# Kernel tuning notes

Measured on AMD Instinct MI355X. Metric: run time of the kernel, lower is better.

## Reference

```python
import jax, jax.numpy as jnp
import numpy as np

B, LQ, LK, D = 8, 2048, 2048, 64
TEMPERATURE = 8.0  # sqrt(D)


def setup_inputs() -> dict:
    key = jax.random.key(0)
    ks = jax.random.split(key, 9)
    q = jax.random.normal(ks[0], (B, LQ, D), dtype=jnp.float32)
    k = jax.random.normal(ks[1], (B, LK, D), dtype=jnp.float32)
    v = jax.random.normal(ks[2], (B, LK, D), dtype=jnp.float32)
    mask = jax.random.randint(ks[3], (B, LQ, LK), 0, 2).astype(jnp.bool_)
    f1 = jax.random.normal(ks[4], (B, LQ, LK), dtype=jnp.float32)
    f2 = jax.random.normal(ks[5], (B, LQ, LK), dtype=jnp.float32)
    f3 = jax.random.normal(ks[6], (B, LQ, LK), dtype=jnp.float32)
    f4 = jax.random.normal(ks[7], (B, LQ, LK), dtype=jnp.float32)
    f5 = jax.random.normal(ks[8], (B, LQ, LK), dtype=jnp.float32)
    return {"q": q, "k": k, "v": v, "mask": mask,
            "tf_f1_features": f1, "tf_f2_features": f2, "tf_f3_features": f3,
            "tf_f4_features": f4, "tf_f5_features": f5}


def reference(q, k, v, mask, tf_f1_features, tf_f2_features, tf_f3_features,
              tf_f4_features, tf_f5_features):
    # scores: [B, Lq, Lk]
    attn = jnp.einsum("bqd,bkd->bqk", q, k)
    attn = attn + tf_f1_features + tf_f2_features + tf_f3_features + tf_f4_features + tf_f5_features
    attn = attn / TEMPERATURE
    attn = jnp.where(mask, -jnp.inf, attn)
    attn = jax.nn.softmax(attn, axis=2)
    # dropout is identity (attn_dropout=0 / eval mode)
    output = jnp.einsum("bqk,bkd->bqd", attn, v)
    return (output, attn)
```

## Files before the change

kernel.cpp:

```cpp
#include <hip/hip_runtime.h>


#define BBn 8
#define LQn 2048
#define LKn 2048
#define DDn 64

typedef _Float16 half8 __attribute__((ext_vector_type(8)));
typedef _Float16 half4 __attribute__((ext_vector_type(4)));
typedef float floatx4 __attribute__((ext_vector_type(4)));
typedef int intx4 __attribute__((ext_vector_type(4)));

__global__ __launch_bounds__(256) void prep_all(
    const float* __restrict__ kp, const float* __restrict__ vp,
    const unsigned* __restrict__ m, _Float16* __restrict__ kh,
    _Float16* __restrict__ vh, int* __restrict__ flag) {
  const int blk = blockIdx.x;
  const int tid = threadIdx.x;
  if (blk < 512) {
    const size_t off = ((size_t)blk * 256 + tid) * 8;
    floatx4 x0 = *(const floatx4*)(kp + off);
    floatx4 x1 = *(const floatx4*)(kp + off + 4);
    half8 h;
#pragma unroll
    for (int i = 0; i < 4; ++i) { h[i] = (_Float16)x0[i]; h[i + 4] = (_Float16)x1[i]; }
    *(half8*)(kh + off) = h;
  } else if (blk < 1024) {
    int fid = (blk - 512) * 256 + tid;
    const int lr  = fid & 15;  fid >>= 4;
    const int lgp = fid & 3;   fid >>= 2;
    const int dt  = fid & 3;   fid >>= 2;
    const int tc  = fid & 1;   fid >>= 1;
    const int kb6 = fid & 31;  fid >>= 5;
    const int b   = fid;
    const float* vbase =
        vp + ((size_t)(b * LKn + kb6 * 64 + tc * 32 + lgp * 8)) * DDn + dt * 16 + lr;
    half8 h;
#pragma unroll
    for (int i = 0; i < 8; ++i) h[i] = (_Float16)vbase[i * DDn];
    const size_t vof =
        ((((((size_t)b * 32 + kb6) * 2 + tc) * 4 + dt) * 4 + lgp) * 16 + lr) * 8;
    *(half8*)(vh + vof) = h;
  } else {
    __shared__ int s_int, s_f32;
    if (tid == 0) { s_int = 1; s_f32 = 1; }
    __syncthreads();
    int oki = 1, okf = 1;
    for (int i = tid; i < 4096; i += 256) {
      unsigned x = m[i];
      oki &= (x <= 1u);
      okf &= (x == 0u || x == 0x3f800000u);
    }
    atomicAnd(&s_int, oki);
    atomicAnd(&s_f32, okf);
    __syncthreads();
    if (tid == 0) *flag = s_int ? 0 : (s_f32 ? 1 : 2);
  }
}

__global__ __launch_bounds__(256) void detect_mask(const unsigned* __restrict__ m,
                                                   int* __restrict__ flag) {
  __shared__ int s_int, s_f32;
  const int tid = threadIdx.x;
  if (tid == 0) { s_int = 1; s_f32 = 1; }
  __syncthreads();
  int oki = 1, okf = 1;
  for (int i = tid; i < 4096; i += 256) {
    unsigned x = m[i];
    oki &= (x <= 1u);
    okf &= (x == 0u || x == 0x3f800000u);
  }
  atomicAnd(&s_int, oki);
  atomicAnd(&s_f32, okf);
  __syncthreads();
  if (tid == 0) *flag = s_int ? 0 : (s_f32 ? 1 : 2);
}

__global__ __launch_bounds__(512, 4) void attn_logits32(
    const float* __restrict__ qp, const _Float16* __restrict__ kh,
    const float* __restrict__ f1, const float* __restrict__ f2,
    const float* __restrict__ f3, const float* __restrict__ f4,
    const float* __restrict__ f5,
    const void* __restrict__ maskp, const int* __restrict__ flag,
    float* __restrict__ attn, float* __restrict__ invl) {
  const int blk = blockIdx.x;
  const int b   = blk >> 6;
  const int q0  = (blk & 63) << 5;
  const int tid = threadIdx.x;
  const int w   = tid >> 6;
  const int l   = tid & 63;
  const int lr  = l & 15;
  const int lgp = l >> 4;
  const int mode = *flag;

  half8 aq[2][2];
#pragma unroll
  for (int t = 0; t < 2; ++t) {
    const float* qrow = qp + ((size_t)(b * LQn + q0 + t * 16 + lr)) * DDn;
#pragma unroll
    for (int dc = 0; dc < 2; ++dc) {
      floatx4 x0 = *(const floatx4*)(qrow + dc * 32 + lgp * 8);
      floatx4 x1 = *(const floatx4*)(qrow + dc * 32 + lgp * 8 + 4);
      half8 h;
#pragma unroll
      for (int i = 0; i < 4; ++i) { h[i] = (_Float16)x0[i]; h[i + 4] = (_Float16)x1[i]; }
      aq[t][dc] = h;
    }
  }

  float lsum[2][4] = {{0.f, 0.f, 0.f, 0.f}, {0.f, 0.f, 0.f, 0.f}};
  const size_t rowbase = (size_t)b * LQn + q0;
  const int t0 = w * 256;

  for (int kb = t0; kb < t0 + 256; kb += 64) {
    floatx4 acc[2][4];
#pragma unroll
    for (int t = 0; t < 2; ++t)
#pragma unroll
      for (int jj = 0; jj < 4; ++jj) acc[t][jj] = (floatx4){0.f, 0.f, 0.f, 0.f};
#pragma unroll
    for (int dc = 0; dc < 2; ++dc) {
#pragma unroll
      for (int jj = 0; jj < 4; ++jj) {
        half8 bk = *(const half8*)(
            kh + ((size_t)(b * LKn + kb + 4 * lr + jj)) * DDn + dc * 32 + lgp * 8);
#pragma unroll
        for (int t = 0; t < 2; ++t)
          acc[t][jj] = __builtin_amdgcn_mfma_f32_16x16x32_f16(aq[t][dc], bk, acc[t][jj], 0, 0, 0);
      }
    }
#pragma unroll
    for (int t = 0; t < 2; ++t) {
#pragma unroll
      for (int r = 0; r < 4; ++r) {
        const int row = t * 16 + lgp * 4 + r;
        const size_t fof = (rowbase + row) * (size_t)LKn + (size_t)(kb + 4 * lr);
        floatx4 v1 = *(const floatx4*)(f1 + fof);
        floatx4 v2 = *(const floatx4*)(f2 + fof);
        floatx4 v3 = *(const floatx4*)(f3 + fof);
        floatx4 v4 = *(const floatx4*)(f4 + fof);
        floatx4 v5 = *(const floatx4*)(f5 + fof);
        int msk[4];
        if (mode == 0) {
          intx4 m4 = *(const intx4*)((const int*)maskp + fof);
          msk[0] = (m4[0] != 0); msk[1] = (m4[1] != 0);
          msk[2] = (m4[2] != 0); msk[3] = (m4[3] != 0);
        } else if (mode == 1) {
          floatx4 m4 = *(const floatx4*)((const float*)maskp + fof);
          msk[0] = (m4[0] != 0.f); msk[1] = (m4[1] != 0.f);
          msk[2] = (m4[2] != 0.f); msk[3] = (m4[3] != 0.f);
        } else {
          unsigned mv = *(const unsigned*)((const unsigned char*)maskp + fof);
          msk[0] = (int)(mv & 0xffu); msk[1] = (int)((mv >> 8) & 0xffu);
          msk[2] = (int)((mv >> 16) & 0xffu); msk[3] = (int)((mv >> 24) & 0xffu);
        }
        floatx4 ev;
#pragma unroll
        for (int jj = 0; jj < 4; ++jj) {
          float lgt = (acc[t][jj][r] + v1[jj] + v2[jj] + v3[jj] + v4[jj] + v5[jj]) * 0.125f;
          float e = msk[jj] ? 0.f : __expf(lgt - 16.f);
          ev[jj] = e;
          lsum[t][r] += e;
        }
        *(floatx4*)(attn + fof) = ev;
      }
    }
  }

#pragma unroll
  for (int off = 1; off < 16; off <<= 1) {
#pragma unroll
    for (int t = 0; t < 2; ++t)
#pragma unroll
      for (int r = 0; r < 4; ++r) lsum[t][r] += __shfl_xor(lsum[t][r], off);
  }
  __shared__ float lds_l[8][32];
  if (lr == 0) {
#pragma unroll
    for (int t = 0; t < 2; ++t)
#pragma unroll
      for (int r = 0; r < 4; ++r) lds_l[w][t * 16 + lgp * 4 + r] = lsum[t][r];
  }
  __syncthreads();
  if (tid < 32) {
    float s = 0.f;
#pragma unroll
    for (int ww = 0; ww < 8; ++ww) s += lds_l[ww][tid];
    invl[rowbase + tid] = 1.0f / s;
  }
}

__global__ __launch_bounds__(256, 4) void attn_pv(
    const _Float16* __restrict__ vh, const float* __restrict__ invl,
    float* __restrict__ attn, float* __restrict__ outp) {
  const int blk = blockIdx.x;
  const int b   = blk >> 7;
  const int q0  = (blk & 127) << 4;
  const int tid = threadIdx.x;
  const int w   = tid >> 6;
  const int l   = tid & 63;
  const int lr  = l & 15;
  const int lgp = l >> 4;

  __shared__ __align__(16) _Float16 p16[4][16][72];
  __shared__ float osum[4][16][64];

  const size_t rowbase = (size_t)b * LQn + q0;
  float il[4];
#pragma unroll
  for (int r = 0; r < 4; ++r) il[r] = invl[rowbase + lgp * 4 + r];

  floatx4 acc[4];
#pragma unroll
  for (int dt = 0; dt < 4; ++dt) acc[dt] = (floatx4){0.f, 0.f, 0.f, 0.f};

  const int t0 = w * 512;
  for (int kb = t0; kb < t0 + 512; kb += 64) {
    const int kb6 = kb >> 6;
#pragma unroll
    for (int r = 0; r < 4; ++r) {
      const int row = lgp * 4 + r;
      const size_t fof = (rowbase + row) * (size_t)LKn + (size_t)(kb + 4 * lr);
      floatx4 e = *(const floatx4*)(attn + fof);
      floatx4 p = e * il[r];
      *(floatx4*)(attn + fof) = p;
      half4 hp;
#pragma unroll
      for (int jj = 0; jj < 4; ++jj) hp[jj] = (_Float16)p[jj];
      *(half4*)(&p16[w][row][4 * lr]) = hp;
    }
    half8 pa[2];
#pragma unroll
    for (int tc = 0; tc < 2; ++tc)
      pa[tc] = *(const half8*)(&p16[w][lr][tc * 32 + lgp * 8]);
#pragma unroll
    for (int tc = 0; tc < 2; ++tc) {
#pragma unroll
      for (int dt = 0; dt < 4; ++dt) {
        half8 bv = *(const half8*)(
            vh + ((((((size_t)b * 32 + kb6) * 2 + tc) * 4 + dt) * 4 + lgp) * 16 + lr) * 8);
        acc[dt] = __builtin_amdgcn_mfma_f32_16x16x32_f16(pa[tc], bv, acc[dt], 0, 0, 0);
      }
    }
  }

#pragma unroll
  for (int dt = 0; dt < 4; ++dt) {
#pragma unroll
    for (int r = 0; r < 4; ++r) osum[w][lgp * 4 + r][dt * 16 + lr] = acc[dt][r];
  }
  __syncthreads();
#pragma unroll
  for (int ii = 0; ii < 4; ++ii) {
    int idx = tid + 256 * ii;
    int row = idx >> 6, d = idx & 63;
    float s = osum[0][row][d] + osum[1][row][d] + osum[2][row][d] + osum[3][row][d];
    outp[(rowbase + row) * DDn + d] = s;
  }
}

__global__ __launch_bounds__(512, 4) void attn_logits_fb(
    const float* __restrict__ qp, const float* __restrict__ kp,
    const float* __restrict__ f1, const float* __restrict__ f2,
    const float* __restrict__ f3, const float* __restrict__ f4,
    const float* __restrict__ f5,
    const void* __restrict__ maskp, const int* __restrict__ flag,
    float* __restrict__ attn, float* __restrict__ invl) {
  const int blk = blockIdx.x;
  const int b   = blk >> 7;
  const int q0  = (blk & 127) << 4;
  const int tid = threadIdx.x;
  const int w   = tid >> 6;
  const int l   = tid & 63;
  const int lr  = l & 15;
  const int lgp = l >> 4;
  const int mode = *flag;
  const float* qrow = qp + ((size_t)(b * LQn + q0 + lr)) * DDn;
  half8 aq[2];
#pragma unroll
  for (int dc = 0; dc < 2; ++dc) {
    floatx4 x0 = *(const floatx4*)(qrow + dc * 32 + lgp * 8);
    floatx4 x1 = *(const floatx4*)(qrow + dc * 32 + lgp * 8 + 4);
    half8 h;
#pragma unroll
    for (int i = 0; i < 4; ++i) { h[i] = (_Float16)x0[i]; h[i + 4] = (_Float16)x1[i]; }
    aq[dc] = h;
  }
  float lsum[4] = {0.f, 0.f, 0.f, 0.f};
  const size_t rowbase = (size_t)b * LQn + q0;
  const int t0 = w * 256;
  for (int kb = t0; kb < t0 + 256; kb += 64) {
    floatx4 acc[4];
#pragma unroll
    for (int jj = 0; jj < 4; ++jj) acc[jj] = (floatx4){0.f, 0.f, 0.f, 0.f};
#pragma unroll
    for (int dc = 0; dc < 2; ++dc) {
#pragma unroll
      for (int jj = 0; jj < 4; ++jj) {
        const float* krow =
            kp + ((size_t)(b * LKn + kb + 4 * lr + jj)) * DDn + dc * 32 + lgp * 8;
        floatx4 x0 = *(const floatx4*)(krow);
        floatx4 x1 = *(const floatx4*)(krow + 4);
        half8 h;
#pragma unroll
        for (int i = 0; i < 4; ++i) { h[i] = (_Float16)x0[i]; h[i + 4] = (_Float16)x1[i]; }
        acc[jj] = __builtin_amdgcn_mfma_f32_16x16x32_f16(aq[dc], h, acc[jj], 0, 0, 0);
      }
    }
#pragma unroll
    for (int r = 0; r < 4; ++r) {
      const int row = lgp * 4 + r;
      const size_t fof = (rowbase + row) * (size_t)LKn + (size_t)(kb + 4 * lr);
      floatx4 v1 = *(const floatx4*)(f1 + fof);
      floatx4 v2 = *(const floatx4*)(f2 + fof);
      floatx4 v3 = *(const floatx4*)(f3 + fof);
      floatx4 v4 = *(const floatx4*)(f4 + fof);
      floatx4 v5 = *(const floatx4*)(f5 + fof);
      int msk[4];
      if (mode == 0) {
        intx4 m4 = *(const intx4*)((const int*)maskp + fof);
        msk[0] = (m4[0] != 0); msk[1] = (m4[1] != 0);
        msk[2] = (m4[2] != 0); msk[3] = (m4[3] != 0);
      } else if (mode == 1) {
        floatx4 m4 = *(const floatx4*)((const float*)maskp + fof);
        msk[0] = (m4[0] != 0.f); msk[1] = (m4[1] != 0.f);
        msk[2] = (m4[2] != 0.f); msk[3] = (m4[3] != 0.f);
      } else {
        unsigned mv = *(const unsigned*)((const unsigned char*)maskp + fof);
        msk[0] = (int)(mv & 0xffu); msk[1] = (int)((mv >> 8) & 0xffu);
        msk[2] = (int)((mv >> 16) & 0xffu); msk[3] = (int)((mv >> 24) & 0xffu);
      }
      floatx4 ev;
#pragma unroll
      for (int jj = 0; jj < 4; ++jj) {
        float lgt = (acc[jj][r] + v1[jj] + v2[jj] + v3[jj] + v4[jj] + v5[jj]) * 0.125f;
        float e = msk[jj] ? 0.f : __expf(lgt - 16.f);
        ev[jj] = e;
        lsum[r] += e;
      }
      *(floatx4*)(attn + fof) = ev;
    }
  }
#pragma unroll
  for (int off = 1; off < 16; off <<= 1) {
#pragma unroll
    for (int r = 0; r < 4; ++r) lsum[r] += __shfl_xor(lsum[r], off);
  }
  __shared__ float lds_l[8][16];
  if (lr == 0) {
#pragma unroll
    for (int r = 0; r < 4; ++r) lds_l[w][lgp * 4 + r] = lsum[r];
  }
  __syncthreads();
  if (tid < 16) {
    float s = 0.f;
#pragma unroll
    for (int ww = 0; ww < 8; ++ww) s += lds_l[ww][tid];
    invl[rowbase + tid] = 1.0f / s;
  }
}

__global__ __launch_bounds__(256, 4) void attn_pv_fb(
    const float* __restrict__ vp, const float* __restrict__ invl,
    float* __restrict__ attn, float* __restrict__ outp) {
  const int blk = blockIdx.x;
  const int b   = blk >> 7;
  const int q0  = (blk & 127) << 4;
  const int tid = threadIdx.x;
  const int w   = tid >> 6;
  const int l   = tid & 63;
  const int lr  = l & 15;
  const int lgp = l >> 4;
  __shared__ __align__(16) _Float16 p16[4][16][72];
  __shared__ float osum[4][16][64];
  const size_t rowbase = (size_t)b * LQn + q0;
  float il[4];
#pragma unroll
  for (int r = 0; r < 4; ++r) il[r] = invl[rowbase + lgp * 4 + r];
  floatx4 acc[4];
#pragma unroll
  for (int dt = 0; dt < 4; ++dt) acc[dt] = (floatx4){0.f, 0.f, 0.f, 0.f};
  const int t0 = w * 512;
  for (int kb = t0; kb < t0 + 512; kb += 64) {
#pragma unroll
    for (int r = 0; r < 4; ++r) {
      const int row = lgp * 4 + r;
      const size_t fof = (rowbase + row) * (size_t)LKn + (size_t)(kb + 4 * lr);
      floatx4 e = *(const floatx4*)(attn + fof);
      floatx4 p = e * il[r];
      *(floatx4*)(attn + fof) = p;
      half4 hp;
#pragma unroll
      for (int jj = 0; jj < 4; ++jj) hp[jj] = (_Float16)p[jj];
      *(half4*)(&p16[w][row][4 * lr]) = hp;
    }
    half8 pa[2];
#pragma unroll
    for (int tc = 0; tc < 2; ++tc)
      pa[tc] = *(const half8*)(&p16[w][lr][tc * 32 + lgp * 8]);
#pragma unroll
    for (int tc = 0; tc < 2; ++tc) {
#pragma unroll
      for (int dt = 0; dt < 4; ++dt) {
        const float* vbase =
            vp + ((size_t)(b * LKn + kb + tc * 32 + lgp * 8)) * DDn + dt * 16 + lr;
        half8 bv;
#pragma unroll
        for (int i = 0; i < 8; ++i) bv[i] = (_Float16)vbase[i * DDn];
        acc[dt] = __builtin_amdgcn_mfma_f32_16x16x32_f16(pa[tc], bv, acc[dt], 0, 0, 0);
      }
    }
  }
#pragma unroll
  for (int dt = 0; dt < 4; ++dt) {
#pragma unroll
    for (int r = 0; r < 4; ++r) osum[w][lgp * 4 + r][dt * 16 + lr] = acc[dt][r];
  }
  __syncthreads();
#pragma unroll
  for (int ii = 0; ii < 4; ++ii) {
    int idx = tid + 256 * ii;
    int row = idx >> 6, d = idx & 63;
    float s = osum[0][row][d] + osum[1][row][d] + osum[2][row][d] + osum[3][row][d];
    outp[(rowbase + row) * DDn + d] = s;
  }
}

extern "C" void kernel_launch(void* const* d_in, const int* in_sizes, int n_in,
                              void* d_out, int out_size, void* d_ws, size_t ws_size,
                              hipStream_t stream) {
  const float* q  = (const float*)d_in[0];
  const float* k  = (const float*)d_in[1];
  const float* v  = (const float*)d_in[2];
  const void*  mask = d_in[3];
  const float* f1 = (const float*)d_in[4];
  const float* f2 = (const float*)d_in[5];
  const float* f3 = (const float*)d_in[6];
  const float* f4 = (const float*)d_in[7];
  const float* f5 = (const float*)d_in[8];

  float* outp = (float*)d_out;
  float* attn = outp + (size_t)BBn * LQn * DDn;

  const size_t KH_OFF = 131072, VH_OFF = KH_OFF + 2097152, NEED = VH_OFF + 2097152;
  float* invl = (float*)d_ws;
  int*   flag = (int*)((char*)d_ws + 65536);
  _Float16* kh = (_Float16*)((char*)d_ws + KH_OFF);
  _Float16* vh = (_Float16*)((char*)d_ws + VH_OFF);

  if (ws_size >= NEED) {
    prep_all<<<1025, 256, 0, stream>>>(k, v, (const unsigned*)mask, kh, vh, flag);
    attn_logits32<<<512, 512, 0, stream>>>(q, kh, f1, f2, f3, f4, f5, mask, flag, attn, invl);
    attn_pv<<<1024, 256, 0, stream>>>(vh, invl, attn, outp);
  } else {
    int* flag2 = (int*)d_ws + (BBn * LQn);
    detect_mask<<<1, 256, 0, stream>>>((const unsigned*)mask, flag2);
    attn_logits_fb<<<1024, 512, 0, stream>>>(q, k, f1, f2, f3, f4, f5, mask, flag2, attn, invl);
    attn_pv_fb<<<1024, 256, 0, stream>>>(v, invl, attn, outp);
  }
}
```

Baseline: 294.5 us.

## Stage unnormalized exponentials in fp16 scratch instead of fp32 attn round-trip

The logits kernel now writes unnormalized exponentials as fp16 to a workspace buffer instead of fp32 into the attn output. The PV kernel reads that half-width buffer, normalizes it, and writes the final fp32 attn once. This removes the fp32 read-modify-write of attn and replaces it with a half-size intermediate. The K fp16 preconversion is dropped in favour of converting K inline, and the logits kernel goes back to 16-row tiles. The shift moves from 16 to 5, and storing the exponentials in fp16 risks overflow or precision loss if logits are large. The path depends on the workspace holding 64MB.

New measurement: 278.3 us. 5.5% less time.

```diff
diff --git a/kernel.cpp b/kernel.cpp
--- a/kernel.cpp
+++ b/kernel.cpp
@@ -11,22 +11,13 @@
 typedef float floatx4 __attribute__((ext_vector_type(4)));
 typedef int intx4 __attribute__((ext_vector_type(4)));
 
-__global__ __launch_bounds__(256) void prep_all(
-    const float* __restrict__ kp, const float* __restrict__ vp,
-    const unsigned* __restrict__ m, _Float16* __restrict__ kh,
+__global__ __launch_bounds__(256) void prep_v(
+    const float* __restrict__ vp, const unsigned* __restrict__ m,
     _Float16* __restrict__ vh, int* __restrict__ flag) {
   const int blk = blockIdx.x;
   const int tid = threadIdx.x;
   if (blk < 512) {
-    const size_t off = ((size_t)blk * 256 + tid) * 8;
-    floatx4 x0 = *(const floatx4*)(kp + off);
-    floatx4 x1 = *(const floatx4*)(kp + off + 4);
-    half8 h;
-#pragma unroll
-    for (int i = 0; i < 4; ++i) { h[i] = (_Float16)x0[i]; h[i + 4] = (_Float16)x1[i]; }
-    *(half8*)(kh + off) = h;
-  } else if (blk < 1024) {
-    int fid = (blk - 512) * 256 + tid;
+    int fid = blk * 256 + tid;
     const int lr  = fid & 15;  fid >>= 4;
     const int lgp = fid & 3;   fid >>= 2;
     const int dt  = fid & 3;   fid >>= 2;
@@ -58,214 +49,13 @@
   }
 }
 
-__global__ __launch_bounds__(256) void detect_mask(const unsigned* __restrict__ m,
-                                                   int* __restrict__ flag) {
-  __shared__ int s_int, s_f32;
-  const int tid = threadIdx.x;
-  if (tid == 0) { s_int = 1; s_f32 = 1; }
-  __syncthreads();
-  int oki = 1, okf = 1;
-  for (int i = tid; i < 4096; i += 256) {
-    unsigned x = m[i];
-    oki &= (x <= 1u);
-    okf &= (x == 0u || x == 0x3f800000u);
-  }
-  atomicAnd(&s_int, oki);
-  atomicAnd(&s_f32, okf);
-  __syncthreads();
-  if (tid == 0) *flag = s_int ? 0 : (s_f32 ? 1 : 2);
-}
-
-__global__ __launch_bounds__(512, 4) void attn_logits32(
-    const float* __restrict__ qp, const _Float16* __restrict__ kh,
-    const float* __restrict__ f1, const float* __restrict__ f2,
-    const float* __restrict__ f3, const float* __restrict__ f4,
-    const float* __restrict__ f5,
-    const void* __restrict__ maskp, const int* __restrict__ flag,
-    float* __restrict__ attn, float* __restrict__ invl) {
-  const int blk = blockIdx.x;
-  const int b   = blk >> 6;
-  const int q0  = (blk & 63) << 5;
-  const int tid = threadIdx.x;
-  const int w   = tid >> 6;
-  const int l   = tid & 63;
-  const int lr  = l & 15;
-  const int lgp = l >> 4;
-  const int mode = *flag;
-
-  half8 aq[2][2];
-#pragma unroll
-  for (int t = 0; t < 2; ++t) {
-    const float* qrow = qp + ((size_t)(b * LQn + q0 + t * 16 + lr)) * DDn;
-#pragma unroll
-    for (int dc = 0; dc < 2; ++dc) {
-      floatx4 x0 = *(const floatx4*)(qrow + dc * 32 + lgp * 8);
-      floatx4 x1 = *(const floatx4*)(qrow + dc * 32 + lgp * 8 + 4);
-      half8 h;
-#pragma unroll
-      for (int i = 0; i < 4; ++i) { h[i] = (_Float16)x0[i]; h[i + 4] = (_Float16)x1[i]; }
-      aq[t][dc] = h;
-    }
-  }
-
-  float lsum[2][4] = {{0.f, 0.f, 0.f, 0.f}, {0.f, 0.f, 0.f, 0.f}};
-  const size_t rowbase = (size_t)b * LQn + q0;
-  const int t0 = w * 256;
-
-  for (int kb = t0; kb < t0 + 256; kb += 64) {
-    floatx4 acc[2][4];
-#pragma unroll
-    for (int t = 0; t < 2; ++t)
-#pragma unroll
-      for (int jj = 0; jj < 4; ++jj) acc[t][jj] = (floatx4){0.f, 0.f, 0.f, 0.f};
-#pragma unroll
-    for (int dc = 0; dc < 2; ++dc) {
-#pragma unroll
-      for (int jj = 0; jj < 4; ++jj) {
-        half8 bk = *(const half8*)(
-            kh + ((size_t)(b * LKn + kb + 4 * lr + jj)) * DDn + dc * 32 + lgp * 8);
-#pragma unroll
-        for (int t = 0; t < 2; ++t)
-          acc[t][jj] = __builtin_amdgcn_mfma_f32_16x16x32_f16(aq[t][dc], bk, acc[t][jj], 0, 0, 0);
-      }
-    }
-#pragma unroll
-    for (int t = 0; t < 2; ++t) {
-#pragma unroll
-      for (int r = 0; r < 4; ++r) {
-        const int row = t * 16 + lgp * 4 + r;
-        const size_t fof = (rowbase + row) * (size_t)LKn + (size_t)(kb + 4 * lr);
-        floatx4 v1 = *(const floatx4*)(f1 + fof);
-        floatx4 v2 = *(const floatx4*)(f2 + fof);
-        floatx4 v3 = *(const floatx4*)(f3 + fof);
-        floatx4 v4 = *(const floatx4*)(f4 + fof);
-        floatx4 v5 = *(const floatx4*)(f5 + fof);
-        int msk[4];
-        if (mode == 0) {
-          intx4 m4 = *(const intx4*)((const int*)maskp + fof);
-          msk[0] = (m4[0] != 0); msk[1] = (m4[1] != 0);
-          msk[2] = (m4[2] != 0); msk[3] = (m4[3] != 0);
-        } else if (mode == 1) {
-          floatx4 m4 = *(const floatx4*)((const float*)maskp + fof);
-          msk[0] = (m4[0] != 0.f); msk[1] = (m4[1] != 0.f);
-          msk[2] = (m4[2] != 0.f); msk[3] = (m4[3] != 0.f);
-        } else {
-          unsigned mv = *(const unsigned*)((const unsigned char*)maskp + fof);
-          msk[0] = (int)(mv & 0xffu); msk[1] = (int)((mv >> 8) & 0xffu);
-          msk[2] = (int)((mv >> 16) & 0xffu); msk[3] = (int)((mv >> 24) & 0xffu);
-        }
-        floatx4 ev;
-#pragma unroll
-        for (int jj = 0; jj < 4; ++jj) {
-          float lgt = (acc[t][jj][r] + v1[jj] + v2[jj] + v3[jj] + v4[jj] + v5[jj]) * 0.125f;
-          float e = msk[jj] ? 0.f : __expf(lgt - 16.f);
-          ev[jj] = e;
-          lsum[t][r] += e;
-        }
-        *(floatx4*)(attn + fof) = ev;
-      }
-    }
-  }
-
-#pragma unroll
-  for (int off = 1; off < 16; off <<= 1) {
-#pragma unroll
-    for (int t = 0; t < 2; ++t)
-#pragma unroll
-      for (int r = 0; r < 4; ++r) lsum[t][r] += __shfl_xor(lsum[t][r], off);
-  }
-  __shared__ float lds_l[8][32];
-  if (lr == 0) {
-#pragma unroll
-    for (int t = 0; t < 2; ++t)
-#pragma unroll
-      for (int r = 0; r < 4; ++r) lds_l[w][t * 16 + lgp * 4 + r] = lsum[t][r];
-  }
-  __syncthreads();
-  if (tid < 32) {
-    float s = 0.f;
-#pragma unroll
-    for (int ww = 0; ww < 8; ++ww) s += lds_l[ww][tid];
-    invl[rowbase + tid] = 1.0f / s;
-  }
-}
-
-__global__ __launch_bounds__(256, 4) void attn_pv(
-    const _Float16* __restrict__ vh, const float* __restrict__ invl,
-    float* __restrict__ attn, float* __restrict__ outp) {
-  const int blk = blockIdx.x;
-  const int b   = blk >> 7;
-  const int q0  = (blk & 127) << 4;
-  const int tid = threadIdx.x;
-  const int w   = tid >> 6;
-  const int l   = tid & 63;
-  const int lr  = l & 15;
-  const int lgp = l >> 4;
-
-  __shared__ __align__(16) _Float16 p16[4][16][72];
-  __shared__ float osum[4][16][64];
-
-  const size_t rowbase = (size_t)b * LQn + q0;
-  float il[4];
-#pragma unroll
-  for (int r = 0; r < 4; ++r) il[r] = invl[rowbase + lgp * 4 + r];
-
-  floatx4 acc[4];
-#pragma unroll
-  for (int dt = 0; dt < 4; ++dt) acc[dt] = (floatx4){0.f, 0.f, 0.f, 0.f};
-
-  const int t0 = w * 512;
-  for (int kb = t0; kb < t0 + 512; kb += 64) {
-    const int kb6 = kb >> 6;
-#pragma unroll
-    for (int r = 0; r < 4; ++r) {
-      const int row = lgp * 4 + r;
-      const size_t fof = (rowbase + row) * (size_t)LKn + (size_t)(kb + 4 * lr);
-      floatx4 e = *(const floatx4*)(attn + fof);
-      floatx4 p = e * il[r];
-      *(floatx4*)(attn + fof) = p;
-      half4 hp;
-#pragma unroll
-      for (int jj = 0; jj < 4; ++jj) hp[jj] = (_Float16)p[jj];
-      *(half4*)(&p16[w][row][4 * lr]) = hp;
-    }
-    half8 pa[2];
-#pragma unroll
-    for (int tc = 0; tc < 2; ++tc)
-      pa[tc] = *(const half8*)(&p16[w][lr][tc * 32 + lgp * 8]);
-#pragma unroll
-    for (int tc = 0; tc < 2; ++tc) {
-#pragma unroll
-      for (int dt = 0; dt < 4; ++dt) {
-        half8 bv = *(const half8*)(
-            vh + ((((((size_t)b * 32 + kb6) * 2 + tc) * 4 + dt) * 4 + lgp) * 16 + lr) * 8);
-        acc[dt] = __builtin_amdgcn_mfma_f32_16x16x32_f16(pa[tc], bv, acc[dt], 0, 0, 0);
-      }
-    }
-  }
-
-#pragma unroll
-  for (int dt = 0; dt < 4; ++dt) {
-#pragma unroll
-    for (int r = 0; r < 4; ++r) osum[w][lgp * 4 + r][dt * 16 + lr] = acc[dt][r];
-  }
-  __syncthreads();
-#pragma unroll
-  for (int ii = 0; ii < 4; ++ii) {
-    int idx = tid + 256 * ii;
-    int row = idx >> 6, d = idx & 63;
-    float s = osum[0][row][d] + osum[1][row][d] + osum[2][row][d] + osum[3][row][d];
-    outp[(rowbase + row) * DDn + d] = s;
-  }
-}
-
-__global__ __launch_bounds__(512, 4) void attn_logits_fb(
+__global__ __launch_bounds__(512, 4) void fused_logits_exp(
     const float* __restrict__ qp, const float* __restrict__ kp,
     const float* __restrict__ f1, const float* __restrict__ f2,
     const float* __restrict__ f3, const float* __restrict__ f4,
     const float* __restrict__ f5,
     const void* __restrict__ maskp, const int* __restrict__ flag,
-    float* __restrict__ attn, float* __restrict__ invl) {
+    _Float16* __restrict__ e16, float* __restrict__ invl) {
   const int blk = blockIdx.x;
   const int b   = blk >> 7;
   const int q0  = (blk & 127) << 4;
@@ -275,6 +65,7 @@
   const int lr  = l & 15;
   const int lgp = l >> 4;
   const int mode = *flag;
+
   const float* qrow = qp + ((size_t)(b * LQn + q0 + lr)) * DDn;
   half8 aq[2];
 #pragma unroll
@@ -286,9 +77,11 @@
     for (int i = 0; i < 4; ++i) { h[i] = (_Float16)x0[i]; h[i + 4] = (_Float16)x1[i]; }
     aq[dc] = h;
   }
+
   float lsum[4] = {0.f, 0.f, 0.f, 0.f};
   const size_t rowbase = (size_t)b * LQn + q0;
   const int t0 = w * 256;
+
   for (int kb = t0; kb < t0 + 256; kb += 64) {
     floatx4 acc[4];
 #pragma unroll
@@ -330,6 +123,182 @@
         msk[0] = (int)(mv & 0xffu); msk[1] = (int)((mv >> 8) & 0xffu);
         msk[2] = (int)((mv >> 16) & 0xffu); msk[3] = (int)((mv >> 24) & 0xffu);
       }
+      half4 hp;
+      float ls = 0.f;
+#pragma unroll
+      for (int jj = 0; jj < 4; ++jj) {
+        float lgt = (acc[jj][r] + v1[jj] + v2[jj] + v3[jj] + v4[jj] + v5[jj]) * 0.125f;
+        float e = msk[jj] ? 0.f : __expf(lgt - 5.f);
+        hp[jj] = (_Float16)e;
+        ls += e;
+      }
+      lsum[r] += ls;
+      *(half4*)(e16 + fof) = hp;
+    }
+  }
+
+#pragma unroll
+  for (int off = 1; off < 16; off <<= 1) {
+#pragma unroll
+    for (int r = 0; r < 4; ++r) lsum[r] += __shfl_xor(lsum[r], off);
+  }
+  __shared__ float lds_l[8][16];
+  if (lr == 0) {
+#pragma unroll
+    for (int r = 0; r < 4; ++r) lds_l[w][lgp * 4 + r] = lsum[r];
+  }
+  __syncthreads();
+  if (tid < 16) {
+    float s = 0.f;
+#pragma unroll
+    for (int ww = 0; ww < 8; ++ww) s += lds_l[ww][tid];
+    invl[rowbase + tid] = 1.0f / s;
+  }
+}
+
+__global__ __launch_bounds__(256, 4) void attn_pv(
+    const _Float16* __restrict__ vh, const float* __restrict__ invl,
+    const _Float16* __restrict__ e16, float* __restrict__ attn,
+    float* __restrict__ outp) {
+  const int blk = blockIdx.x;
+  const int b   = blk >> 7;
+  const int q0  = (blk & 127) << 4;
+  const int tid = threadIdx.x;
+  const int w   = tid >> 6;
+  const int l   = tid & 63;
+  const int lr  = l & 15;
+  const int lgp = l >> 4;
+
+  __shared__ __align__(16) _Float16 p16[4][16][72];
+  __shared__ float osum[4][16][64];
+
+  const size_t rowbase = (size_t)b * LQn + q0;
+  float il[4];
+#pragma unroll
+  for (int r = 0; r < 4; ++r) il[r] = invl[rowbase + lgp * 4 + r];
+
+  floatx4 acc[4];
+#pragma unroll
+  for (int dt = 0; dt < 4; ++dt) acc[dt] = (floatx4){0.f, 0.f, 0.f, 0.f};
+
+  const int t0 = w * 512;
+  for (int kb = t0; kb < t0 + 512; kb += 64) {
+    const int kb6 = kb >> 6;
+#pragma unroll
+    for (int r = 0; r < 4; ++r) {
+      const int row = lgp * 4 + r;
+      const size_t fof = (rowbase + row) * (size_t)LKn + (size_t)(kb + 4 * lr);
+      half4 h = *(const half4*)(e16 + fof);
+      floatx4 p;
+#pragma unroll
+      for (int jj = 0; jj < 4; ++jj) p[jj] = (float)h[jj] * il[r];
+      *(floatx4*)(attn + fof) = p;
+      half4 hp;
+#pragma unroll
+      for (int jj = 0; jj < 4; ++jj) hp[jj] = (_Float16)p[jj];
+      *(half4*)(&p16[w][row][4 * lr]) = hp;
+    }
+    half8 pa[2];
+#pragma unroll
+    for (int tc = 0; tc < 2; ++tc)
+      pa[tc] = *(const half8*)(&p16[w][lr][tc * 32 + lgp * 8]);
+#pragma unroll
+    for (int tc = 0; tc < 2; ++tc) {
+#pragma unroll
+      for (int dt = 0; dt < 4; ++dt) {
+        half8 bv = *(const half8*)(
+            vh + ((((((size_t)b * 32 + kb6) * 2 + tc) * 4 + dt) * 4 + lgp) * 16 + lr) * 8);
+        acc[dt] = __builtin_amdgcn_mfma_f32_16x16x32_f16(pa[tc], bv, acc[dt], 0, 0, 0);
+      }
+    }
+  }
+
+#pragma unroll
+  for (int dt = 0; dt < 4; ++dt) {
+#pragma unroll
+    for (int r = 0; r < 4; ++r) osum[w][lgp * 4 + r][dt * 16 + lr] = acc[dt][r];
+  }
+  __syncthreads();
+#pragma unroll
+  for (int ii = 0; ii < 4; ++ii) {
+    int idx = tid + 256 * ii;
+    int row = idx >> 6, d = idx & 63;
+    float s = osum[0][row][d] + osum[1][row][d] + osum[2][row][d] + osum[3][row][d];
+    outp[(rowbase + row) * DDn + d] = s;
+  }
+}
+
+__global__ __launch_bounds__(512, 4) void fused_logits_exp_fb(
+    const float* __restrict__ qp, const float* __restrict__ kp,
+    const float* __restrict__ f1, const float* __restrict__ f2,
+    const float* __restrict__ f3, const float* __restrict__ f4,
+    const float* __restrict__ f5,
+    const void* __restrict__ maskp, const int* __restrict__ flag,
+    float* __restrict__ attn, float* __restrict__ invl) {
+  const int blk = blockIdx.x;
+  const int b   = blk >> 7;
+  const int q0  = (blk & 127) << 4;
+  const int tid = threadIdx.x;
+  const int w   = tid >> 6;
+  const int l   = tid & 63;
+  const int lr  = l & 15;
+  const int lgp = l >> 4;
+  const int mode = *flag;
+  const float* qrow = qp + ((size_t)(b * LQn + q0 + lr)) * DDn;
+  half8 aq[2];
+#pragma unroll
+  for (int dc = 0; dc < 2; ++dc) {
+    floatx4 x0 = *(const floatx4*)(qrow + dc * 32 + lgp * 8);
+    floatx4 x1 = *(const floatx4*)(qrow + dc * 32 + lgp * 8 + 4);
+    half8 h;
+#pragma unroll
+    for (int i = 0; i < 4; ++i) { h[i] = (_Float16)x0[i]; h[i + 4] = (_Float16)x1[i]; }
+    aq[dc] = h;
+  }
+  float lsum[4] = {0.f, 0.f, 0.f, 0.f};
+  const size_t rowbase = (size_t)b * LQn + q0;
+  const int t0 = w * 256;
+  for (int kb = t0; kb < t0 + 256; kb += 64) {
+    floatx4 acc[4];
+#pragma unroll
+    for (int jj = 0; jj < 4; ++jj) acc[jj] = (floatx4){0.f, 0.f, 0.f, 0.f};
+#pragma unroll
+    for (int dc = 0; dc < 2; ++dc) {
+#pragma unroll
+      for (int jj = 0; jj < 4; ++jj) {
+        const float* krow =
+            kp + ((size_t)(b * LKn + kb + 4 * lr + jj)) * DDn + dc * 32 + lgp * 8;
+        floatx4 x0 = *(const floatx4*)(krow);
+        floatx4 x1 = *(const floatx4*)(krow + 4);
+        half8 h;
+#pragma unroll
+        for (int i = 0; i < 4; ++i) { h[i] = (_Float16)x0[i]; h[i + 4] = (_Float16)x1[i]; }
+        acc[jj] = __builtin_amdgcn_mfma_f32_16x16x32_f16(aq[dc], h, acc[jj], 0, 0, 0);
+      }
+    }
+#pragma unroll
+    for (int r = 0; r < 4; ++r) {
+      const int row = lgp * 4 + r;
+      const size_t fof = (rowbase + row) * (size_t)LKn + (size_t)(kb + 4 * lr);
+      floatx4 v1 = *(const floatx4*)(f1 + fof);
+      floatx4 v2 = *(const floatx4*)(f2 + fof);
+      floatx4 v3 = *(const floatx4*)(f3 + fof);
+      floatx4 v4 = *(const floatx4*)(f4 + fof);
+      floatx4 v5 = *(const floatx4*)(f5 + fof);
+      int msk[4];
+      if (mode == 0) {
+        intx4 m4 = *(const intx4*)((const int*)maskp + fof);
+        msk[0] = (m4[0] != 0); msk[1] = (m4[1] != 0);
+        msk[2] = (m4[2] != 0); msk[3] = (m4[3] != 0);
+      } else if (mode == 1) {
+        floatx4 m4 = *(const floatx4*)((const float*)maskp + fof);
+        msk[0] = (m4[0] != 0.f); msk[1] = (m4[1] != 0.f);
+        msk[2] = (m4[2] != 0.f); msk[3] = (m4[3] != 0.f);
+      } else {
+        unsigned mv = *(const unsigned*)((const unsigned char*)maskp + fof);
+        msk[0] = (int)(mv & 0xffu); msk[1] = (int)((mv >> 8) & 0xffu);
+        msk[2] = (int)((mv >> 16) & 0xffu); msk[3] = (int)((mv >> 24) & 0xffu);
+      }
       floatx4 ev;
 #pragma unroll
       for (int jj = 0; jj < 4; ++jj) {
@@ -361,7 +330,7 @@
 }
 
 __global__ __launch_bounds__(256, 4) void attn_pv_fb(
-    const float* __restrict__ vp, const float* __restrict__ invl,
+    const _Float16* __restrict__ vh, const float* __restrict__ invl,
     float* __restrict__ attn, float* __restrict__ outp) {
   const int blk = blockIdx.x;
   const int b   = blk >> 7;
@@ -372,7 +341,7 @@
   const int lr  = l & 15;
   const int lgp = l >> 4;
   __shared__ __align__(16) _Float16 p16[4][16][72];
-  __shared__ float osum[4][16][64];
+  __shared__ float osum2[4][16][64];
   const size_t rowbase = (size_t)b * LQn + q0;
   float il[4];
 #pragma unroll
@@ -382,6 +351,7 @@
   for (int dt = 0; dt < 4; ++dt) acc[dt] = (floatx4){0.f, 0.f, 0.f, 0.f};
   const int t0 = w * 512;
   for (int kb = t0; kb < t0 + 512; kb += 64) {
+    const int kb6 = kb >> 6;
 #pragma unroll
     for (int r = 0; r < 4; ++r) {
       const int row = lgp * 4 + r;
@@ -402,11 +372,8 @@
     for (int tc = 0; tc < 2; ++tc) {
 #pragma unroll
       for (int dt = 0; dt < 4; ++dt) {
-        const float* vbase =
-            vp + ((size_t)(b * LKn + kb + tc * 32 + lgp * 8)) * DDn + dt * 16 + lr;
-        half8 bv;
-#pragma unroll
-        for (int i = 0; i < 8; ++i) bv[i] = (_Float16)vbase[i * DDn];
+        half8 bv = *(const half8*)(
+            vh + ((((((size_t)b * 32 + kb6) * 2 + tc) * 4 + dt) * 4 + lgp) * 16 + lr) * 8);
         acc[dt] = __builtin_amdgcn_mfma_f32_16x16x32_f16(pa[tc], bv, acc[dt], 0, 0, 0);
       }
     }
@@ -414,14 +381,14 @@
 #pragma unroll
   for (int dt = 0; dt < 4; ++dt) {
 #pragma unroll
-    for (int r = 0; r < 4; ++r) osum[w][lgp * 4 + r][dt * 16 + lr] = acc[dt][r];
+    for (int r = 0; r < 4; ++r) osum2[w][lgp * 4 + r][dt * 16 + lr] = acc[dt][r];
   }
   __syncthreads();
 #pragma unroll
   for (int ii = 0; ii < 4; ++ii) {
     int idx = tid + 256 * ii;
     int row = idx >> 6, d = idx & 63;
-    float s = osum[0][row][d] + osum[1][row][d] + osum[2][row][d] + osum[3][row][d];
+    float s = osum2[0][row][d] + osum2[1][row][d] + osum2[2][row][d] + osum2[3][row][d];
     outp[(rowbase + row) * DDn + d] = s;
   }
 }
@@ -442,20 +409,24 @@
   float* outp = (float*)d_out;
   float* attn = outp + (size_t)BBn * LQn * DDn;
 
-  const size_t KH_OFF = 131072, VH_OFF = KH_OFF + 2097152, NEED = VH_OFF + 2097152;
+  const size_t VH_OFF = 131072;
+  const size_t E16_OFF = VH_OFF + 2097152;
+  const size_t E16_BYTES = (size_t)BBn * LQn * LKn * 2;
+  const size_t NEED16 = E16_OFF + E16_BYTES;
   float* invl = (float*)d_ws;
   int*   flag = (int*)((char*)d_ws + 65536);
-  _Float16* kh = (_Float16*)((char*)d_ws + KH_OFF);
-  _Float16* vh = (_Float16*)((char*)d_ws + VH_OFF);
-
-  if (ws_size >= NEED) {
-    prep_all<<<1025, 256, 0, stream>>>(k, v, (const unsigned*)mask, kh, vh, flag);
-    attn_logits32<<<512, 512, 0, stream>>>(q, kh, f1, f2, f3, f4, f5, mask, flag, attn, invl);
-    attn_pv<<<1024, 256, 0, stream>>>(vh, invl, attn, outp);
+  _Float16* vh  = (_Float16*)((char*)d_ws + VH_OFF);
+  _Float16* e16 = (_Float16*)((char*)d_ws + E16_OFF);
+  const int use16 = (ws_size >= NEED16) ? 1 : 0;
+
+  prep_v<<<513, 256, 0, stream>>>(v, (const unsigned*)mask, vh, flag);
+  if (use16) {
+    fused_logits_exp<<<1024, 512, 0, stream>>>(q, k, f1, f2, f3, f4, f5,
+                                               mask, flag, e16, invl);
+    attn_pv<<<1024, 256, 0, stream>>>(vh, invl, e16, attn, outp);
   } else {
-    int* flag2 = (int*)d_ws + (BBn * LQn);
-    detect_mask<<<1, 256, 0, stream>>>((const unsigned*)mask, flag2);
-    attn_logits_fb<<<1024, 512, 0, stream>>>(q, k, f1, f2, f3, f4, f5, mask, flag2, attn, invl);
-    attn_pv_fb<<<1024, 256, 0, stream>>>(v, invl, attn, outp);
-  }
-}
+    fused_logits_exp_fb<<<1024, 512, 0, stream>>>(q, k, f1, f2, f3, f4, f5,
+                                                  mask, flag, attn, invl);
+    attn_pv_fb<<<1024, 256, 0, stream>>>(vh, invl, attn, outp);
+  }
+}
```
